# Kernel optimization log

Hardware: AMD Instinct MI355X
Metric: run time of the kernel (lower is better)

Reference implementation:

```python
import jax, jax.numpy as jnp
import numpy as np

H = 16  # n_heads (from init_kwargs)


def l2norm(x, eps=1e-6):
    return x * jax.lax.rsqrt(jnp.sum(x * x, axis=-1, keepdims=True) + eps)


def causal_conv1d(x, w, b):
    # depthwise causal conv: x (B,T,D), w (D,k), b (D,). Matches torch
    # Conv1d(d,d,k,groups=d,padding=k-1) followed by [:, :, :T] truncation.
    T = x.shape[1]
    k = w.shape[1]
    xp = jnp.pad(x, ((0, 0), (k - 1, 0), (0, 0)))
    y = b
    for j in range(k):  # k=4 taps, fixed small loop
        y = y + xp[:, j:j + T, :] * w[:, j]
    return y


def setup_inputs():
    key = jax.random.key(0)
    ks = jax.random.split(key, 16)
    B, T, D, kc = 2, 2048, 1024, 4
    d = D // H
    s = 1.0 / np.sqrt(D)
    return {
        "x": jax.random.normal(ks[0], (B, T, D), jnp.float32),
        "Wq": jax.random.normal(ks[1], (D, D), jnp.float32) * s,
        "Wk": jax.random.normal(ks[2], (D, D), jnp.float32) * s,
        "Wv": jax.random.normal(ks[3], (D, D), jnp.float32) * s,
        "Wo": jax.random.normal(ks[4], (D, D), jnp.float32) * s,
        "Wg": jax.random.normal(ks[5], (D, D), jnp.float32) * s,
        "Wb": jax.random.normal(ks[6], (D, H), jnp.float32) * s,
        "cq_w": jax.random.normal(ks[7], (D, kc), jnp.float32) * 0.3,
        "cq_b": jax.random.normal(ks[8], (D,), jnp.float32) * 0.1,
        "ck_w": jax.random.normal(ks[9], (D, kc), jnp.float32) * 0.3,
        "ck_b": jax.random.normal(ks[10], (D,), jnp.float32) * 0.1,
        "cv_w": jax.random.normal(ks[11], (D, kc), jnp.float32) * 0.3,
        "cv_b": jax.random.normal(ks[12], (D,), jnp.float32) * 0.1,
        "nw": jnp.ones((d,), jnp.float32),
    }


def reference(x, Wq, Wk, Wv, Wo, Wg, Wb, cq_w, cq_b, ck_w, ck_b, cv_w, cv_b, nw):
    B, T, D = x.shape
    d = D // H
    q = l2norm(jax.nn.silu(causal_conv1d(x @ Wq, cq_w, cq_b)).reshape(B, T, H, d))
    q = q / jnp.sqrt(jnp.asarray(d, x.dtype))
    k = l2norm(jax.nn.silu(causal_conv1d(x @ Wk, ck_w, ck_b)).reshape(B, T, H, d))
    v = jax.nn.silu(causal_conv1d(x @ Wv, cv_w, cv_b)).reshape(B, T, H, d)
    gate = (x @ Wg).reshape(B, T, H, d)
    beta = jax.nn.sigmoid(x @ Wb)[..., None]  # (B,T,H,1)

    def step(S, qkvb):
        q_t, k_t, v_t, b_t = qkvb  # (B,H,d), (B,H,d), (B,H,d), (B,H,1)
        err = (v_t - jnp.einsum('bhk,bhkv->bhv', k_t, S)) * b_t
        S = S + jnp.einsum('bhk,bhv->bhkv', k_t, err)
        o_t = jnp.einsum('bhk,bhkv->bhv', q_t, S)
        return S, o_t

    S0 = jnp.zeros((B, H, d, d), x.dtype)
    xs = (q.transpose(1, 0, 2, 3), k.transpose(1, 0, 2, 3),
          v.transpose(1, 0, 2, 3), beta.transpose(1, 0, 2, 3))
    _, oT = jax.lax.scan(step, S0, xs)
    o = oT.transpose(1, 0, 2, 3)  # (B,T,H,d)
    # RMSNorm over head_dim
    o = o * jax.lax.rsqrt(jnp.mean(o * o, axis=-1, keepdims=True) + 1e-5) * nw
    o = o * jax.nn.silu(gate)
    return o.reshape(B, T, D) @ Wo
```

## Files before the change

kernel.cpp:

```cpp
#include <hip/hip_runtime.h>
#include <hip/hip_bf16.h>

typedef __attribute__((ext_vector_type(8))) short short8;
typedef __attribute__((ext_vector_type(4))) float f32x4;

#define TSEQ 2048
#define DMODEL 1024
#define NH 16
#define HD 64
#define PLANE 4194304

__device__ __forceinline__ ushort f2bf(float f) {
    union { float f; unsigned int u; } c; c.f = f;
    unsigned int u = c.u + 0x7fffu + ((c.u >> 16) & 1u);
    return (ushort)(u >> 16);
}

__device__ __forceinline__ float bf2f(ushort u) {
    union { unsigned int i; float f; } c; c.i = ((unsigned int)u) << 16;
    return c.f;
}

__device__ __forceinline__ void split2(float x, ushort& h, ushort& l) {
    h = f2bf(x);
    float r = x - bf2f(h);
    l = f2bf(r);
}

__device__ __forceinline__ float silu_f(float y) {
    return y / (1.f + __expf(-y));
}

__device__ __forceinline__ void gl_lds16(const float* g, float* l) {
    __builtin_amdgcn_global_load_lds(
        (__attribute__((address_space(1))) void*)g,
        (__attribute__((address_space(3))) void*)l, 16, 0, 0);
}
__device__ __forceinline__ void gl_lds16u(const ushort* g, ushort* l) {
    __builtin_amdgcn_global_load_lds(
        (__attribute__((address_space(1))) void*)g,
        (__attribute__((address_space(3))) void*)l, 16, 0, 0);
}

__global__ void gdn_cvt_x(const float* __restrict__ x, ushort* __restrict__ xb) {
    int i = blockIdx.x * 256 + threadIdx.x;
    float4 v = ((const float4*)x)[i];
    ushort4 o;
    o.x = f2bf(v.x); o.y = f2bf(v.y); o.z = f2bf(v.z); o.w = f2bf(v.w);
    ((ushort4*)xb)[i] = o;
}

__global__ void gdn_cvt_w(const float* __restrict__ Wq, const float* __restrict__ Wk,
                          const float* __restrict__ Wv, const float* __restrict__ Wg,
                          const float* __restrict__ Wo, ushort* __restrict__ wt) {
    __shared__ float tile[32][33];
    int z = blockIdx.z;
    const float* W = (z == 0) ? Wq : (z == 1) ? Wk : (z == 2) ? Wv : (z == 3) ? Wg : Wo;
    int n0 = blockIdx.x * 32, k0 = blockIdx.y * 32;
    int tx = threadIdx.x, ty = threadIdx.y;
    #pragma unroll
    for (int j = 0; j < 32; j += 8)
        tile[ty + j][tx] = W[(size_t)(k0 + ty + j) * DMODEL + n0 + tx];
    __syncthreads();
    ushort* o = wt + (size_t)z * DMODEL * DMODEL;
    #pragma unroll
    for (int j = 0; j < 32; j += 8)
        o[(size_t)(n0 + ty + j) * DMODEL + k0 + tx] = f2bf(tile[tx][ty + j]);
}

__global__ void gdn_beta(const float* __restrict__ x, const float* __restrict__ Wb,
                         float* __restrict__ betaT) {
    __shared__ float xs[16][DMODEL];
    int tid = threadIdx.x;
    int m0 = blockIdx.x * 16;
    #pragma unroll
    for (int i = 0; i < 16; i++) {
        int idx = i * 256 + tid;
        int row = idx >> 8, c4 = idx & 255;
        *(float4*)&xs[row][c4 * 4] =
            *(const float4*)&x[(size_t)(m0 + row) * DMODEL + c4 * 4];
    }
    __syncthreads();
    int h = tid & 15, mi = tid >> 4;
    float acc = 0.f;
    for (int k = 0; k < DMODEL; ++k)
        acc += xs[mi][k] * Wb[k * NH + h];
    int m = m0 + mi;
    int b = m >> 11, t = m & (TSEQ - 1);
    betaT[((b * NH + h) << 11) + t] = 1.f / (1.f + __expf(-acc));
}

#define BK 32
__global__ __launch_bounds__(256) void gdn_gemm(const ushort* __restrict__ A,
                                                const ushort* __restrict__ Bt,
                                                float* __restrict__ outF,
                                                size_t planeStride) {
    __shared__ ushort As[128 * BK];
    __shared__ ushort Bs[128 * BK];
    int tid = threadIdx.x;
    int lane = tid & 63, wid = tid >> 6;
    int wm = wid & 1, wn = wid >> 1;
    int l15 = lane & 15, quad = lane >> 4;
    int bm = blockIdx.x, bn = blockIdx.y;
    const int K = DMODEL;

    int e0 = wid, e1 = wid + 4;
    int srow0 = e0 * 16 + (lane >> 2), srow1 = e1 * 16 + (lane >> 2);
    int scol = (lane & 3) * 8;
    const ushort* Ag0 = A + (size_t)(bm * 128 + srow0) * K + scol;
    const ushort* Ag1 = A + (size_t)(bm * 128 + srow1) * K + scol;
    const ushort* Bg0 = Bt + (size_t)(bn * 128 + srow0) * K + scol;
    const ushort* Bg1 = Bt + (size_t)(bn * 128 + srow1) * K + scol;
    ushort* Al0 = As + e0 * 512;
    ushort* Al1 = As + e1 * 512;
    ushort* Bl0 = Bs + e0 * 512;
    ushort* Bl1 = Bs + e1 * 512;

    f32x4 acc[4][4];
    #pragma unroll
    for (int i = 0; i < 4; i++)
        #pragma unroll
        for (int j = 0; j < 4; j++)
            acc[i][j] = (f32x4){0.f, 0.f, 0.f, 0.f};

    for (int kt = 0; kt < K; kt += BK) {
        __syncthreads();
        gl_lds16u(Ag0 + kt, Al0);
        gl_lds16u(Ag1 + kt, Al1);
        gl_lds16u(Bg0 + kt, Bl0);
        gl_lds16u(Bg1 + kt, Bl1);
        __syncthreads();
        short8 af[4], bf[4];
        #pragma unroll
        for (int i = 0; i < 4; i++) {
            af[i] = *(const short8*)&As[(wm * 64 + i * 16 + l15) * BK + quad * 8];
            bf[i] = *(const short8*)&Bs[(wn * 64 + i * 16 + l15) * BK + quad * 8];
        }
        #pragma unroll
        for (int mt = 0; mt < 4; mt++)
            #pragma unroll
            for (int nt = 0; nt < 4; nt++)
                acc[mt][nt] = __builtin_amdgcn_mfma_f32_16x16x32_bf16(
                    af[mt], bf[nt], acc[mt][nt], 0, 0, 0);
    }

    #pragma unroll
    for (int mt = 0; mt < 4; mt++)
        #pragma unroll
        for (int nt = 0; nt < 4; nt++)
            #pragma unroll
            for (int r = 0; r < 4; r++) {
                int row = bm * 128 + wm * 64 + mt * 16 + quad * 4 + r;
                int col = bn * 128 + wn * 64 + nt * 16 + l15;
                outF[(size_t)(col >> 10) * planeStride + (size_t)row * 1024 + (col & 1023)]
                    = acc[mt][nt][r];
            }
}

__global__ void gdn_conv(const float* __restrict__ pre,
                         const float* __restrict__ cqw, const float* __restrict__ cqb,
                         const float* __restrict__ ckw, const float* __restrict__ ckb,
                         const float* __restrict__ cvw, const float* __restrict__ cvb,
                         float* __restrict__ qn, float* __restrict__ kn, float* __restrict__ vn) {
    int m = blockIdx.x;
    int which = blockIdx.y;
    int t = m & (TSEQ - 1);
    const float* cw = (which == 0) ? cqw : (which == 1) ? ckw : cvw;
    const float* cb = (which == 0) ? cqb : (which == 1) ? ckb : cvb;
    float* dst = (which == 0) ? qn : (which == 1) ? kn : vn;
    int c = threadIdx.x * 4;

    float w[4][4];
    #pragma unroll
    for (int i = 0; i < 4; i++) {
        float4 t4 = ((const float4*)cw)[c + i];
        w[i][0] = t4.x; w[i][1] = t4.y; w[i][2] = t4.z; w[i][3] = t4.w;
    }
    float4 bias = ((const float4*)cb)[threadIdx.x];
    float y[4] = {bias.x, bias.y, bias.z, bias.w};

    const float* src = pre + (size_t)which * PLANE + (size_t)m * DMODEL + c;
    #pragma unroll
    for (int j = 0; j < 4; j++) {
        int tt = t - 3 + j;
        if (tt >= 0) {
            float4 xv = *(const float4*)(src + (long)(j - 3) * DMODEL);
            y[0] += xv.x * w[0][j];
            y[1] += xv.y * w[1][j];
            y[2] += xv.z * w[2][j];
            y[3] += xv.w * w[3][j];
        }
    }
    #pragma unroll
    for (int i = 0; i < 4; i++) y[i] = silu_f(y[i]);

    if (which < 2) {
        float ss = y[0]*y[0] + y[1]*y[1] + y[2]*y[2] + y[3]*y[3];
        ss += __shfl_xor(ss, 1);
        ss += __shfl_xor(ss, 2);
        ss += __shfl_xor(ss, 4);
        ss += __shfl_xor(ss, 8);
        float sc = rsqrtf(ss + 1e-6f);
        if (which == 0) sc *= 0.125f;
        #pragma unroll
        for (int i = 0; i < 4; i++) y[i] *= sc;
    }
    float4 o; o.x = y[0]; o.y = y[1]; o.z = y[2]; o.w = y[3];
    ((float4*)(dst + (size_t)m * 1024))[threadIdx.x] = o;
}

__global__ __launch_bounds__(256) void gdn_chunk(
    const float* __restrict__ kn, const float* __restrict__ vn,
    const float* __restrict__ betaT,
    ushort* __restrict__ WTst, ushort* __restrict__ U0st,
    float* __restrict__ Pst, float* __restrict__ Rst)
{
    __shared__ ushort Khi[64 * 72], Klo[64 * 72];
    __shared__ ushort KThi[64 * 72], KTlo[64 * 72];
    __shared__ ushort XThi[128 * 72], XTlo[128 * 72];
    __shared__ ushort Mneghi[64 * 72], Mneglo[64 * 72];
    __shared__ float  Xf[64 * 132];
    __shared__ float  MmDiag[4 * 16 * 20];
    __shared__ float  bet[64];

    int c = blockIdx.x, bh = blockIdx.y;
    int b = bh >> 4, h = bh & 15;
    int tid = threadIdx.x;
    int w = tid >> 6, lane = tid & 63;
    int l15 = lane & 15, quad = lane >> 4;
    size_t gbase = ((size_t)(b * TSEQ + c * 64)) * DMODEL + h * 64;
    size_t u = (size_t)bh * 32 + c;

    if (tid < 64) bet[tid] = betaT[((size_t)bh << 11) + c * 64 + tid];
    #pragma unroll
    for (int i = 0; i < 18; i++) {
        ((uint*)XThi)[tid + 256 * i] = 0u;
        ((uint*)XTlo)[tid + 256 * i] = 0u;
    }
    __syncthreads();

    #pragma unroll
    for (int i = 0; i < 4; i++) {
        int idx = tid + 256 * i;
        int r = idx >> 4, c4 = (idx & 15) * 4;
        float4 kv = *(const float4*)&kn[gbase + (size_t)r * DMODEL + c4];
        float4 vv = *(const float4*)&vn[gbase + (size_t)r * DMODEL + c4];
        float br = bet[r];
        float4 xk; xk.x = br * kv.x; xk.y = br * kv.y; xk.z = br * kv.z; xk.w = br * kv.w;
        float4 xv; xv.x = br * vv.x; xv.y = br * vv.y; xv.z = br * vv.z; xv.w = br * vv.w;
        *(float4*)&Xf[r * 132 + c4] = xk;
        *(float4*)&Xf[r * 132 + 64 + c4] = xv;
        ushort h0, l0, h1, l1, h2, l2, h3, l3;
        split2(kv.x, h0, l0); split2(kv.y, h1, l1);
        split2(kv.z, h2, l2); split2(kv.w, h3, l3);
        ((uint*)&Khi[r * 72 + c4])[0] = (uint)h0 | ((uint)h1 << 16);
        ((uint*)&Khi[r * 72 + c4])[1] = (uint)h2 | ((uint)h3 << 16);
        ((uint*)&Klo[r * 72 + c4])[0] = (uint)l0 | ((uint)l1 << 16);
        ((uint*)&Klo[r * 72 + c4])[1] = (uint)l2 | ((uint)l3 << 16);
        KThi[(c4 + 0) * 72 + r] = h0; KThi[(c4 + 1) * 72 + r] = h1;
        KThi[(c4 + 2) * 72 + r] = h2; KThi[(c4 + 3) * 72 + r] = h3;
        KTlo[(c4 + 0) * 72 + r] = l0; KTlo[(c4 + 1) * 72 + r] = l1;
        KTlo[(c4 + 2) * 72 + r] = l2; KTlo[(c4 + 3) * 72 + r] = l3;
    }
    __syncthreads();

    {
        f32x4 mAcc[4];
        #pragma unroll
        for (int tn = 0; tn < 4; tn++) mAcc[tn] = (f32x4){0.f, 0.f, 0.f, 0.f};
        #pragma unroll
        for (int ks = 0; ks < 2; ks++) {
            short8 aH = *(const short8*)&Khi[(16 * w + l15) * 72 + ks * 32 + quad * 8];
            short8 aL = *(const short8*)&Klo[(16 * w + l15) * 72 + ks * 32 + quad * 8];
            #pragma unroll
            for (int tn = 0; tn < 4; tn++) {
                short8 bH = *(const short8*)&Khi[(16 * tn + l15) * 72 + ks * 32 + quad * 8];
                short8 bL = *(const short8*)&Klo[(16 * tn + l15) * 72 + ks * 32 + quad * 8];
                mAcc[tn] = __builtin_amdgcn_mfma_f32_16x16x32_bf16(aH, bH, mAcc[tn], 0, 0, 0);
                mAcc[tn] = __builtin_amdgcn_mfma_f32_16x16x32_bf16(aH, bL, mAcc[tn], 0, 0, 0);
                mAcc[tn] = __builtin_amdgcn_mfma_f32_16x16x32_bf16(aL, bH, mAcc[tn], 0, 0, 0);
            }
        }
        #pragma unroll
        for (int tn = 0; tn < 4; tn++) {
            #pragma unroll
            for (int r = 0; r < 4; r++) {
                int row = 16 * w + quad * 4 + r;
                int col = tn * 16 + l15;
                float val = mAcc[tn][r] * bet[row];
                ushort hh = 0, ll = 0;
                if (col < row) {
                    float nv = -val;
                    hh = f2bf(nv);
                    ll = f2bf(nv - bf2f(hh));
                }
                Mneghi[row * 72 + col] = hh;
                Mneglo[row * 72 + col] = ll;
                if (tn == w) MmDiag[w * 320 + (row & 15) * 20 + l15] = val;
            }
        }
    }
    __syncthreads();

    #pragma unroll 1
    for (int st = 0; st < 4; st++) {
        int tb = st * 16;
        if (st) {
            f32x4 acc2[2];
            #pragma unroll
            for (int e = 0; e < 2; e++) {
                int tn = 2 * w + e;
                #pragma unroll
                for (int r = 0; r < 4; r++)
                    acc2[e][r] = Xf[(tb + quad * 4 + r) * 132 + tn * 16 + l15];
            }
            #pragma unroll
            for (int ks = 0; ks < 2; ks++) {
                short8 aH = *(const short8*)&Mneghi[(tb + l15) * 72 + ks * 32 + quad * 8];
                short8 aL = *(const short8*)&Mneglo[(tb + l15) * 72 + ks * 32 + quad * 8];
                #pragma unroll
                for (int e = 0; e < 2; e++) {
                    int tn = 2 * w + e;
                    short8 bH = *(const short8*)&XThi[(tn * 16 + l15) * 72 + ks * 32 + quad * 8];
                    short8 bL = *(const short8*)&XTlo[(tn * 16 + l15) * 72 + ks * 32 + quad * 8];
                    acc2[e] = __builtin_amdgcn_mfma_f32_16x16x32_bf16(aH, bH, acc2[e], 0, 0, 0);
                    acc2[e] = __builtin_amdgcn_mfma_f32_16x16x32_bf16(aH, bL, acc2[e], 0, 0, 0);
                    acc2[e] = __builtin_amdgcn_mfma_f32_16x16x32_bf16(aL, bH, acc2[e], 0, 0, 0);
                }
            }
            #pragma unroll
            for (int e = 0; e < 2; e++) {
                int tn = 2 * w + e;
                #pragma unroll
                for (int r = 0; r < 4; r++)
                    Xf[(tb + quad * 4 + r) * 132 + tn * 16 + l15] = acc2[e][r];
            }
        }
        __syncthreads();

        if (tid < 128) {
            const int j = tid;
            const float* MD = &MmDiag[st * 320];
            float xr[16];
            #pragma unroll
            for (int sb = 0; sb < 4; sb++) {
                float b4[4];
                #pragma unroll
                for (int i = 0; i < 4; i++)
                    b4[i] = Xf[(tb + sb * 4 + i) * 132 + j];
                #pragma unroll
                for (int u4 = 0; u4 < sb; u4++) {
                    #pragma unroll
                    for (int i = 0; i < 4; i++) {
                        float4 m4 = *(const float4*)&MD[(sb * 4 + i) * 20 + u4 * 4];
                        b4[i] -= m4.x * xr[u4 * 4 + 0] + m4.y * xr[u4 * 4 + 1]
                               + m4.z * xr[u4 * 4 + 2] + m4.w * xr[u4 * 4 + 3];
                    }
                }
                float x0 = b4[0];
                float x1 = b4[1] - MD[(sb * 4 + 1) * 20 + sb * 4 + 0] * x0;
                float x2 = b4[2] - MD[(sb * 4 + 2) * 20 + sb * 4 + 0] * x0
                                 - MD[(sb * 4 + 2) * 20 + sb * 4 + 1] * x1;
                float x3 = b4[3] - MD[(sb * 4 + 3) * 20 + sb * 4 + 0] * x0
                                 - MD[(sb * 4 + 3) * 20 + sb * 4 + 1] * x1
                                 - MD[(sb * 4 + 3) * 20 + sb * 4 + 2] * x2;
                xr[sb * 4 + 0] = x0; xr[sb * 4 + 1] = x1;
                xr[sb * 4 + 2] = x2; xr[sb * 4 + 3] = x3;
            }
            ushort hs[16], ls[16];
            #pragma unroll
            for (int i = 0; i < 16; i++) split2(xr[i], hs[i], ls[i]);
            uint4 ph0, ph1, pl0, pl1;
            ph0.x = (uint)hs[0] | ((uint)hs[1] << 16);  ph0.y = (uint)hs[2] | ((uint)hs[3] << 16);
            ph0.z = (uint)hs[4] | ((uint)hs[5] << 16);  ph0.w = (uint)hs[6] | ((uint)hs[7] << 16);
            ph1.x = (uint)hs[8] | ((uint)hs[9] << 16);  ph1.y = (uint)hs[10] | ((uint)hs[11] << 16);
            ph1.z = (uint)hs[12] | ((uint)hs[13] << 16); ph1.w = (uint)hs[14] | ((uint)hs[15] << 16);
            pl0.x = (uint)ls[0] | ((uint)ls[1] << 16);  pl0.y = (uint)ls[2] | ((uint)ls[3] << 16);
            pl0.z = (uint)ls[4] | ((uint)ls[5] << 16);  pl0.w = (uint)ls[6] | ((uint)ls[7] << 16);
            pl1.x = (uint)ls[8] | ((uint)ls[9] << 16);  pl1.y = (uint)ls[10] | ((uint)ls[11] << 16);
            pl1.z = (uint)ls[12] | ((uint)ls[13] << 16); pl1.w = (uint)ls[14] | ((uint)ls[15] << 16);
            *(uint4*)&XThi[j * 72 + tb] = ph0;  *(uint4*)&XThi[j * 72 + tb + 8] = ph1;
            *(uint4*)&XTlo[j * 72 + tb] = pl0;  *(uint4*)&XTlo[j * 72 + tb + 8] = pl1;
            if (j < 64) {
                ushort* wdst = WTst + u * 4096 + j * 64 + tb;
                *(uint4*)wdst = ph0; *(uint4*)(wdst + 8) = ph1;
            } else {
                ushort* udst = U0st + u * 4096 + (size_t)tb * 64 + (j - 64);
                #pragma unroll
                for (int i = 0; i < 16; i++) udst[i * 64] = hs[i];
            }
        }
        __syncthreads();
    }

    {
        f32x4 pAcc[4], rAcc[4];
        #pragma unroll
        for (int tn = 0; tn < 4; tn++) {
            pAcc[tn] = (f32x4){0.f, 0.f, 0.f, 0.f};
            rAcc[tn] = (f32x4){0.f, 0.f, 0.f, 0.f};
        }
        #pragma unroll
        for (int ks = 0; ks < 2; ks++) {
            short8 aH = *(const short8*)&XThi[(16 * w + l15) * 72 + ks * 32 + quad * 8];
            short8 aL = *(const short8*)&XTlo[(16 * w + l15) * 72 + ks * 32 + quad * 8];
            short8 cH = *(const short8*)&KThi[(16 * w + l15) * 72 + ks * 32 + quad * 8];
            short8 cL = *(const short8*)&KTlo[(16 * w + l15) * 72 + ks * 32 + quad * 8];
            #pragma unroll
            for (int tn = 0; tn < 4; tn++) {
                short8 bH = *(const short8*)&KThi[(16 * tn + l15) * 72 + ks * 32 + quad * 8];
                short8 bL = *(const short8*)&KTlo[(16 * tn + l15) * 72 + ks * 32 + quad * 8];
                pAcc[tn] = __builtin_amdgcn_mfma_f32_16x16x32_bf16(aH, bH, pAcc[tn], 0, 0, 0);
                pAcc[tn] = __builtin_amdgcn_mfma_f32_16x16x32_bf16(aH, bL, pAcc[tn], 0, 0, 0);
                pAcc[tn] = __builtin_amdgcn_mfma_f32_16x16x32_bf16(aL, bH, pAcc[tn], 0, 0, 0);
                short8 uH = *(const short8*)&XThi[(64 + 16 * tn + l15) * 72 + ks * 32 + quad * 8];
                short8 uL = *(const short8*)&XTlo[(64 + 16 * tn + l15) * 72 + ks * 32 + quad * 8];
                rAcc[tn] = __builtin_amdgcn_mfma_f32_16x16x32_bf16(cH, uH, rAcc[tn], 0, 0, 0);
                rAcc[tn] = __builtin_amdgcn_mfma_f32_16x16x32_bf16(cH, uL, rAcc[tn], 0, 0, 0);
                rAcc[tn] = __builtin_amdgcn_mfma_f32_16x16x32_bf16(cL, uH, rAcc[tn], 0, 0, 0);
            }
        }
        float* Po = Pst + u * 4096;
        float* Ro = Rst + u * 4096;
        #pragma unroll
        for (int tn = 0; tn < 4; tn++) {
            #pragma unroll
            for (int r = 0; r < 4; r++) {
                int row = 16 * w + quad * 4 + r;
                int col = tn * 16 + l15;
                Po[row * 64 + col] = pAcc[tn][r];
                Ro[col * 64 + row] = rAcc[tn][r];
            }
        }
    }
}

__global__ __launch_bounds__(256) void gdn_sstep(const float* __restrict__ Pst,
                                                 const float* __restrict__ Rst,
                                                 float* __restrict__ S0st)
{
    __shared__ float PTl[3][4096];
    __shared__ float Rl[3][1024];
    __shared__ float SshT[2][16][72];

    int bh = blockIdx.x >> 2, cg = blockIdx.x & 3;
    int tid = threadIdx.x;
    int t0 = (tid & 15) * 4;
    int j  = tid >> 4;
    int jg = cg * 16 + j;
    int wv = tid >> 6, ln = tid & 63;

    size_t ubase = (size_t)bh * 32 * 4096;

    *(float4*)&SshT[0][j][t0] = (float4){0.f, 0.f, 0.f, 0.f};

    #pragma unroll
    for (int t = 0; t < 2; t++) {
        size_t ub = ubase + (size_t)t * 4096;
        #pragma unroll
        for (int q = 0; q < 4; q++)
            gl_lds16(Pst + ub + (wv * 4 + q) * 256 + ln * 4, &PTl[t][(wv * 4 + q) * 256]);
        gl_lds16(Rst + ub + cg * 1024 + wv * 256 + ln * 4, &Rl[t][wv * 256]);
    }
    asm volatile("s_waitcnt vmcnt(5)" ::: "memory");
    asm volatile("s_waitcnt lgkmcnt(0)" ::: "memory");
    __builtin_amdgcn_s_barrier();

    int cur3 = 0;
    #pragma unroll 1
    for (int c = 0; c < 32; ++c) {
        int cur = c & 1, nxt = cur ^ 1;
        if (c + 2 < 32) {
            int b3 = cur3 + 2; if (b3 >= 3) b3 -= 3;
            size_t ub2 = ubase + (size_t)(c + 2) * 4096;
            #pragma unroll
            for (int q = 0; q < 4; q++)
                gl_lds16(Pst + ub2 + (wv * 4 + q) * 256 + ln * 4, &PTl[b3][(wv * 4 + q) * 256]);
            gl_lds16(Rst + ub2 + cg * 1024 + wv * 256 + ln * 4, &Rl[b3][wv * 256]);
        }
        float4 sold = *(const float4*)&SshT[cur][j][t0];
        size_t ub = ubase + (size_t)c * 4096;
        S0st[ub + (size_t)(t0 + 0) * 64 + jg] = sold.x;
        S0st[ub + (size_t)(t0 + 1) * 64 + jg] = sold.y;
        S0st[ub + (size_t)(t0 + 2) * 64 + jg] = sold.z;
        S0st[ub + (size_t)(t0 + 3) * 64 + jg] = sold.w;
        float4 racc = *(const float4*)&Rl[cur3][j * 64 + t0];
        float sub0 = 0.f, sub1 = 0.f, sub2 = 0.f, sub3 = 0.f;
        #pragma unroll
        for (int u4 = 0; u4 < 16; u4++) {
            float4 sv = *(const float4*)&SshT[cur][j][u4 * 4];
            #pragma unroll
            for (int e = 0; e < 4; e++) {
                float4 pt = *(const float4*)&PTl[cur3][(u4 * 4 + e) * 64 + t0];
                float s1 = (e == 0) ? sv.x : (e == 1) ? sv.y : (e == 2) ? sv.z : sv.w;
                sub0 = fmaf(pt.x, s1, sub0);
                sub1 = fmaf(pt.y, s1, sub1);
                sub2 = fmaf(pt.z, s1, sub2);
                sub3 = fmaf(pt.w, s1, sub3);
            }
        }
        float4 snew;
        snew.x = sold.x + racc.x - sub0;
        snew.y = sold.y + racc.y - sub1;
        snew.z = sold.z + racc.z - sub2;
        snew.w = sold.w + racc.w - sub3;
        *(float4*)&SshT[nxt][j][t0] = snew;
        if (c == 0)       { asm volatile("s_waitcnt vmcnt(9)"  ::: "memory"); }
        else if (c < 30)  { asm volatile("s_waitcnt vmcnt(13)" ::: "memory"); }
        else if (c == 30) { asm volatile("s_waitcnt vmcnt(8)"  ::: "memory"); }
        asm volatile("s_waitcnt lgkmcnt(0)" ::: "memory");
        __builtin_amdgcn_s_barrier();
        cur3 += 1; if (cur3 >= 3) cur3 -= 3;
    }
}

__global__ __launch_bounds__(256) void gdn_opass(
    const float* __restrict__ qn, const float* __restrict__ kn,
    const float* __restrict__ S0st, const ushort* __restrict__ WTst,
    const ushort* __restrict__ U0st, float* __restrict__ otmp2)
{
    __shared__ ushort pool[36864];
    ushort* Qhi  = pool;
    ushort* Qlo  = pool + 4608;
    ushort* Khi  = pool + 2 * 4608;
    ushort* Klo  = pool + 3 * 4608;
    ushort* SThi = pool + 4 * 4608;
    ushort* STlo = pool + 5 * 4608;
    ushort* Wn   = pool + 6 * 4608;
    ushort* Uu   = pool + 7 * 4608;
    ushort* Ghi  = Qhi;  ushort* Glo  = Qlo;
    ushort* EThi = Khi;  ushort* ETlo = Klo;

    int c = blockIdx.x, bh = blockIdx.y;
    int b = bh >> 4, h = bh & 15;
    int tid = threadIdx.x;
    int w = tid >> 6, lane = tid & 63;
    int l15 = lane & 15, quad = lane >> 4;
    size_t gbase = ((size_t)(b * TSEQ + c * 64)) * DMODEL + h * 64;
    size_t u = (size_t)bh * 32 + c;

    #pragma unroll
    for (int i = 0; i < 4; i++) {
        int idx = tid + 256 * i;
        int r = idx >> 4, c4 = (idx & 15) * 4;
        float4 qv = *(const float4*)&qn[gbase + (size_t)r * DMODEL + c4];
        float4 kv = *(const float4*)&kn[gbase + (size_t)r * DMODEL + c4];
        float4 sv = *(const float4*)&S0st[u * 4096 + (size_t)idx * 4];
        ushort h0, l0, h1, l1, h2, l2, h3, l3;
        split2(qv.x, h0, l0); split2(qv.y, h1, l1);
        split2(qv.z, h2, l2); split2(qv.w, h3, l3);
        ((uint*)&Qhi[r * 72 + c4])[0] = (uint)h0 | ((uint)h1 << 16);
        ((uint*)&Qhi[r * 72 + c4])[1] = (uint)h2 | ((uint)h3 << 16);
        ((uint*)&Qlo[r * 72 + c4])[0] = (uint)l0 | ((uint)l1 << 16);
        ((uint*)&Qlo[r * 72 + c4])[1] = (uint)l2 | ((uint)l3 << 16);
        split2(kv.x, h0, l0); split2(kv.y, h1, l1);
        split2(kv.z, h2, l2); split2(kv.w, h3, l3);
        ((uint*)&Khi[r * 72 + c4])[0] = (uint)h0 | ((uint)h1 << 16);
        ((uint*)&Khi[r * 72 + c4])[1] = (uint)h2 | ((uint)h3 << 16);
        ((uint*)&Klo[r * 72 + c4])[0] = (uint)l0 | ((uint)l1 << 16);
        ((uint*)&Klo[r * 72 + c4])[1] = (uint)l2 | ((uint)l3 << 16);
        split2(sv.x, h0, l0); split2(sv.y, h1, l1);
        split2(sv.z, h2, l2); split2(sv.w, h3, l3);
        SThi[(c4 + 0) * 72 + r] = h0; STlo[(c4 + 0) * 72 + r] = l0;
        SThi[(c4 + 1) * 72 + r] = h1; STlo[(c4 + 1) * 72 + r] = l1;
        SThi[(c4 + 2) * 72 + r] = h2; STlo[(c4 + 2) * 72 + r] = l2;
        SThi[(c4 + 3) * 72 + r] = h3; STlo[(c4 + 3) * 72 + r] = l3;
    }
    #pragma unroll
    for (int i = 0; i < 2; i++) {
        int idx = tid + 256 * i;
        uint4 w8 = ((const uint4*)(WTst + u * 4096))[idx];
        int ur = idx >> 3, t8 = (idx & 7) * 8;
        uint v0 = w8.x ^ 0x80008000u, v1 = w8.y ^ 0x80008000u;
        uint v2 = w8.z ^ 0x80008000u, v3 = w8.w ^ 0x80008000u;
        Wn[(t8 + 0) * 72 + ur] = (ushort)v0; Wn[(t8 + 1) * 72 + ur] = (ushort)(v0 >> 16);
        Wn[(t8 + 2) * 72 + ur] = (ushort)v1; Wn[(t8 + 3) * 72 + ur] = (ushort)(v1 >> 16);
        Wn[(t8 + 4) * 72 + ur] = (ushort)v2; Wn[(t8 + 5) * 72 + ur] = (ushort)(v2 >> 16);
        Wn[(t8 + 6) * 72 + ur] = (ushort)v3; Wn[(t8 + 7) * 72 + ur] = (ushort)(v3 >> 16);
        ((uint4*)Uu)[idx] = ((const uint4*)(U0st + u * 4096))[idx];
    }
    __syncthreads();

    f32x4 accG[4], accO[4], accE[4];
    #pragma unroll
    for (int tn = 0; tn < 4; tn++) {
        accG[tn] = (f32x4){0.f, 0.f, 0.f, 0.f};
        accO[tn] = (f32x4){0.f, 0.f, 0.f, 0.f};
        #pragma unroll
        for (int r = 0; r < 4; r++)
            accE[tn][r] = bf2f(Uu[(16 * w + quad * 4 + r) * 64 + tn * 16 + l15]);
    }
    #pragma unroll
    for (int ks = 0; ks < 2; ks++) {
        int ko = ks * 32 + quad * 8;
        short8 qH = *(const short8*)&Qhi[(16 * w + l15) * 72 + ko];
        short8 qL = *(const short8*)&Qlo[(16 * w + l15) * 72 + ko];
        short8 wA = *(const short8*)&Wn [(16 * w + l15) * 72 + ko];
        #pragma unroll
        for (int tn = 0; tn < 4; tn++) {
            short8 kH = *(const short8*)&Khi [(16 * tn + l15) * 72 + ko];
            short8 kL = *(const short8*)&Klo [(16 * tn + l15) * 72 + ko];
            short8 sH = *(const short8*)&SThi[(16 * tn + l15) * 72 + ko];
            short8 sL = *(const short8*)&STlo[(16 * tn + l15) * 72 + ko];
            accG[tn] = __builtin_amdgcn_mfma_f32_16x16x32_bf16(qH, kH, accG[tn], 0, 0, 0);
            accG[tn] = __builtin_amdgcn_mfma_f32_16x16x32_bf16(qH, kL, accG[tn], 0, 0, 0);
            accG[tn] = __builtin_amdgcn_mfma_f32_16x16x32_bf16(qL, kH, accG[tn], 0, 0, 0);
            accO[tn] = __builtin_amdgcn_mfma_f32_16x16x32_bf16(qH, sH, accO[tn], 0, 0, 0);
            accO[tn] = __builtin_amdgcn_mfma_f32_16x16x32_bf16(qH, sL, accO[tn], 0, 0, 0);
            accO[tn] = __builtin_amdgcn_mfma_f32_16x16x32_bf16(qL, sH, accO[tn], 0, 0, 0);
            accE[tn] = __builtin_amdgcn_mfma_f32_16x16x32_bf16(wA, sH, accE[tn], 0, 0, 0);
            accE[tn] = __builtin_amdgcn_mfma_f32_16x16x32_bf16(wA, sL, accE[tn], 0, 0, 0);
        }
    }
    __syncthreads();

    #pragma unroll
    for (int tn = 0; tn < 4; tn++) {
        #pragma unroll
        for (int r = 0; r < 4; r++) {
            int row = 16 * w + quad * 4 + r;
            int col = tn * 16 + l15;
            float gv = (col <= row) ? accG[tn][r] : 0.f;
            ushort gh, gl; split2(gv, gh, gl);
            Ghi[row * 72 + col] = gh; Glo[row * 72 + col] = gl;
            ushort eh, el; split2(accE[tn][r], eh, el);
            EThi[col * 72 + row] = eh; ETlo[col * 72 + row] = el;
        }
    }
    __syncthreads();

    #pragma unroll
    for (int ks = 0; ks < 2; ks++) {
        int ko = ks * 32 + quad * 8;
        short8 gH = *(const short8*)&Ghi[(16 * w + l15) * 72 + ko];
        short8 gL = *(const short8*)&Glo[(16 * w + l15) * 72 + ko];
        #pragma unroll
        for (int tn = 0; tn < 4; tn++) {
            short8 eH = *(const short8*)&EThi[(16 * tn + l15) * 72 + ko];
            short8 eL = *(const short8*)&ETlo[(16 * tn + l15) * 72 + ko];
            accO[tn] = __builtin_amdgcn_mfma_f32_16x16x32_bf16(gH, eH, accO[tn], 0, 0, 0);
            accO[tn] = __builtin_amdgcn_mfma_f32_16x16x32_bf16(gH, eL, accO[tn], 0, 0, 0);
            accO[tn] = __builtin_amdgcn_mfma_f32_16x16x32_bf16(gL, eH, accO[tn], 0, 0, 0);
        }
    }

    #pragma unroll
    for (int tn = 0; tn < 4; tn++) {
        #pragma unroll
        for (int r = 0; r < 4; r++) {
            int row = 16 * w + quad * 4 + r;
            int col = tn * 16 + l15;
            otmp2[(((size_t)bh * 16 + (col >> 2)) * TSEQ + c * 64 + row) * 4 + (col & 3)]
                = accO[tn][r];
        }
    }
}

__global__ void gdn_fuse(const float* __restrict__ otmp2, const float* __restrict__ pre,
                         const float* __restrict__ nw, ushort* __restrict__ ofused) {
    int m = blockIdx.x;
    int b = m >> 11, t = m & (TSEQ - 1);
    int tid = threadIdx.x;
    float4 o = ((const float4*)otmp2)[((size_t)((b * NH + (tid >> 4)) * 16 + (tid & 15))) * TSEQ + t];
    float ss = o.x*o.x + o.y*o.y + o.z*o.z + o.w*o.w;
    ss += __shfl_xor(ss, 1);
    ss += __shfl_xor(ss, 2);
    ss += __shfl_xor(ss, 4);
    ss += __shfl_xor(ss, 8);
    float r = rsqrtf(ss * (1.f / 64.f) + 1e-5f);
    float4 nwv = ((const float4*)nw)[tid & 15];
    float4 g = ((const float4*)(pre + 3 * (size_t)PLANE + (size_t)m * DMODEL))[tid];
    ushort4 out;
    out.x = f2bf(o.x * r * nwv.x * silu_f(g.x));
    out.y = f2bf(o.y * r * nwv.y * silu_f(g.y));
    out.z = f2bf(o.z * r * nwv.z * silu_f(g.z));
    out.w = f2bf(o.w * r * nwv.w * silu_f(g.w));
    ((ushort4*)ofused)[m * 256 + tid] = out;
}

extern "C" void kernel_launch(void* const* d_in, const int* in_sizes, int n_in,
                              void* d_out, int out_size, void* d_ws, size_t ws_size,
                              hipStream_t stream) {
    const float* x    = (const float*)d_in[0];
    const float* Wq   = (const float*)d_in[1];
    const float* Wk   = (const float*)d_in[2];
    const float* Wv   = (const float*)d_in[3];
    const float* Wo   = (const float*)d_in[4];
    const float* Wg   = (const float*)d_in[5];
    const float* Wb   = (const float*)d_in[6];
    const float* cq_w = (const float*)d_in[7];
    const float* cq_b = (const float*)d_in[8];
    const float* ck_w = (const float*)d_in[9];
    const float* ck_b = (const float*)d_in[10];
    const float* cv_w = (const float*)d_in[11];
    const float* cv_b = (const float*)d_in[12];
    const float* nw   = (const float*)d_in[13];

    char* ws = (char*)d_ws;
    ushort* xb     = (ushort*)(ws);
    ushort* wt     = (ushort*)(ws + 8388608);
    float*  pre    = (float*)(ws + 18874368);
    float*  qn     = (float*)(ws + 85983232);
    float*  kn     = (float*)(ws + 102760448);
    float*  vn     = (float*)(ws + 119537664);
    float*  betaT  = (float*)(ws + 136314880);
    float*  otmp2  = (float*)(ws + 136577024);
    ushort* ofused = (ushort*)(ws + 153354240);

    float*  Pst  = pre;
    float*  Rst  = pre + PLANE;
    float*  S0st = pre + 2 * PLANE;
    ushort* WTst = xb;
    ushort* U0st = ofused;

    gdn_cvt_x<<<4096, 256, 0, stream>>>(x, xb);
    gdn_cvt_w<<<dim3(32, 32, 5), dim3(32, 8), 0, stream>>>(Wq, Wk, Wv, Wg, Wo, wt);
    gdn_beta<<<256, 256, 0, stream>>>(x, Wb, betaT);
    gdn_gemm<<<dim3(32, 32), 256, 0, stream>>>(xb, wt, pre, (size_t)PLANE);
    gdn_conv<<<dim3(4096, 3), 256, 0, stream>>>(pre, cq_w, cq_b, ck_w, ck_b, cv_w, cv_b,
                                                qn, kn, vn);
    gdn_chunk<<<dim3(32, 32), 256, 0, stream>>>(kn, vn, betaT, WTst, U0st, Pst, Rst);
    gdn_sstep<<<128, 256, 0, stream>>>(Pst, Rst, S0st);
    gdn_opass<<<dim3(32, 32), 256, 0, stream>>>(qn, kn, S0st, WTst, U0st, otmp2);
    gdn_fuse<<<4096, 256, 0, stream>>>(otmp2, pre, nw, ofused);
    gdn_gemm<<<dim3(32, 8), 256, 0, stream>>>(ofused, wt + 4 * 1024 * 1024,
                                              (float*)d_out, (size_t)0);
}
```

Before: 392.9 us.

## Use 256x256 tiled GEMM with triple-buffered LDS for input projection

Adds a new GEMM kernel with 256x256 output tiles, 512 threads (8 waves, each computing 128x64), and a three-stage LDS pipeline that prefetches two K-steps ahead using direct global-to-LDS loads. It replaces the 128x128 GEMM for the fused Q/K/V/G projection. The larger tile raises arithmetic intensity and cuts redundant global loads. In exchange it launches only 256 blocks, which may underfill the 256 CUs, and the bigger accumulator footprint raises register pressure.

```diff
diff --git a/kernel.cpp b/kernel.cpp
--- a/kernel.cpp
+++ b/kernel.cpp
@@ -154,6 +154,90 @@
                 int col = bn * 128 + wn * 64 + nt * 16 + l15;
                 outF[(size_t)(col >> 10) * planeStride + (size_t)row * 1024 + (col & 1023)]
                     = acc[mt][nt][r];
+            }
+}
+
+__global__ __launch_bounds__(512, 2) void gdn_gemm256(const ushort* __restrict__ A,
+                                                      const ushort* __restrict__ Bt,
+                                                      float* __restrict__ outF,
+                                                      size_t planeStride) {
+    __shared__ ushort As[3][256 * BK];
+    __shared__ ushort Bs[3][256 * BK];
+    int tid = threadIdx.x;
+    int lane = tid & 63, wid = tid >> 6;
+    int wm = wid >> 2, wn = wid & 3;
+    int l15 = lane & 15, quad = lane >> 4;
+    int bm = blockIdx.x, bn = blockIdx.y;
+    const int K = DMODEL;
+
+    int e0 = wid * 2, e1 = wid * 2 + 1;
+    int srow0 = e0 * 16 + (lane >> 2), srow1 = e1 * 16 + (lane >> 2);
+    int scol = (lane & 3) * 8;
+    const ushort* Ag0 = A + (size_t)(bm * 256 + srow0) * K + scol;
+    const ushort* Ag1 = A + (size_t)(bm * 256 + srow1) * K + scol;
+    const ushort* Bg0 = Bt + (size_t)(bn * 256 + srow0) * K + scol;
+    const ushort* Bg1 = Bt + (size_t)(bn * 256 + srow1) * K + scol;
+
+    f32x4 acc[8][4];
+    #pragma unroll
+    for (int i = 0; i < 8; i++)
+        #pragma unroll
+        for (int j = 0; j < 4; j++)
+            acc[i][j] = (f32x4){0.f, 0.f, 0.f, 0.f};
+
+    #pragma unroll
+    for (int t = 0; t < 2; t++) {
+        gl_lds16u(Ag0 + t * BK, &As[t][e0 * 512]);
+        gl_lds16u(Ag1 + t * BK, &As[t][e1 * 512]);
+        gl_lds16u(Bg0 + t * BK, &Bs[t][e0 * 512]);
+        gl_lds16u(Bg1 + t * BK, &Bs[t][e1 * 512]);
+    }
+    asm volatile("s_waitcnt vmcnt(4)" ::: "memory");
+    __builtin_amdgcn_s_barrier();
+
+    #pragma unroll 1
+    for (int c = 0; c < 32; ++c) {
+        if (c + 2 < 32) {
+            int s2 = (c + 2) % 3;
+            int kt2 = (c + 2) * BK;
+            gl_lds16u(Ag0 + kt2, &As[s2][e0 * 512]);
+            gl_lds16u(Ag1 + kt2, &As[s2][e1 * 512]);
+            gl_lds16u(Bg0 + kt2, &Bs[s2][e0 * 512]);
+            gl_lds16u(Bg1 + kt2, &Bs[s2][e1 * 512]);
+        }
+        int cs = c % 3;
+        short8 af[8], bf[4];
+        #pragma unroll
+        for (int mi = 0; mi < 8; mi++)
+            af[mi] = *(const short8*)&As[cs][(wm * 128 + mi * 16 + l15) * BK + quad * 8];
+        #pragma unroll
+        for (int ni = 0; ni < 4; ni++)
+            bf[ni] = *(const short8*)&Bs[cs][(wn * 64 + ni * 16 + l15) * BK + quad * 8];
+        #pragma unroll
+        for (int mi = 0; mi < 8; mi++)
+            #pragma unroll
+            for (int ni = 0; ni < 4; ni++)
+                acc[mi][ni] = __builtin_amdgcn_mfma_f32_16x16x32_bf16(
+                    af[mi], bf[ni], acc[mi][ni], 0, 0, 0);
+        if (c < 30) {
+            asm volatile("s_waitcnt vmcnt(4)" ::: "memory");
+            __builtin_amdgcn_s_barrier();
+        } else if (c == 30) {
+            asm volatile("s_waitcnt vmcnt(0)" ::: "memory");
+            __builtin_amdgcn_s_barrier();
+        }
+    }
+
+    #pragma unroll
+    for (int mi = 0; mi < 8; mi++)
+        #pragma unroll
+        for (int ni = 0; ni < 4; ni++)
+            #pragma unroll
+            for (int r = 0; r < 4; r++) {
+                int row = bm * 256 + wm * 128 + mi * 16 + quad * 4 + r;
+                int col = bn * 256 + wn * 64 + ni * 16 + l15;
+                outF[(size_t)(col >> 10) * planeStride + (size_t)row * 1024 + (col & 1023)]
+                    = acc[mi][ni][r];
             }
 }
 
@@ -716,7 +800,7 @@
     gdn_cvt_x<<<4096, 256, 0, stream>>>(x, xb);
     gdn_cvt_w<<<dim3(32, 32, 5), dim3(32, 8), 0, stream>>>(Wq, Wk, Wv, Wg, Wo, wt);
     gdn_beta<<<256, 256, 0, stream>>>(x, Wb, betaT);
-    gdn_gemm<<<dim3(32, 32), 256, 0, stream>>>(xb, wt, pre, (size_t)PLANE);
+    gdn_gemm256<<<dim3(16, 16), 512, 0, stream>>>(xb, wt, pre, (size_t)PLANE);
     gdn_conv<<<dim3(4096, 3), 256, 0, stream>>>(pre, cq_w, cq_b, ck_w, ck_b, cv_w, cv_b,
                                                 qn, kn, vn);
     gdn_chunk<<<dim3(32, 32), 256, 0, stream>>>(kn, vn, betaT, WTst, U0st, Pst, Rst);
```

Result: no change. 393.2 us (+0.1%).
